# Performance work log

Measured on AMD Instinct MI355X. Metric: run time of the kernel, lower is better.

## Reference

```python
import jax, jax.numpy as jnp
import numpy as np

BATCH = 1024
INPUT_DIM = 4096
HIDDEN_DIM = 4096
N_BLOCKS = 8
BLOCK_SIZE = HIDDEN_DIM // N_BLOCKS          # 512
IN_BLOCK_SIZE = INPUT_DIM // N_BLOCKS        # 512


def setup_inputs() -> dict:
    key = jax.random.key(0)
    ks = jax.random.split(key, 6)
    scale = 1.0 / np.sqrt(BLOCK_SIZE)  # torch GRUCell init: U(-1/sqrt(hidden), 1/sqrt(hidden))
    return {
        "x": jax.random.normal(ks[0], (BATCH, INPUT_DIM), dtype=jnp.float32),
        "h": jax.random.normal(ks[1], (BATCH, HIDDEN_DIM), dtype=jnp.float32),
        "W_ih": jax.random.normal(ks[2], (N_BLOCKS, 3 * BLOCK_SIZE, IN_BLOCK_SIZE), dtype=jnp.float32) * scale,
        "W_hh": jax.random.normal(ks[3], (N_BLOCKS, 3 * BLOCK_SIZE, BLOCK_SIZE), dtype=jnp.float32) * scale,
        "b_ih": jax.random.normal(ks[4], (N_BLOCKS, 3 * BLOCK_SIZE), dtype=jnp.float32) * scale,
        "b_hh": jax.random.normal(ks[5], (N_BLOCKS, 3 * BLOCK_SIZE), dtype=jnp.float32) * scale,
    }


def reference(x, h, W_ih, W_hh, b_ih, b_hh):
    B = x.shape[0]
    n, g3, ibs = W_ih.shape           # n_blocks, 3*block_size, input_block_size
    bs = W_hh.shape[2]                # block_size
    xb = x.reshape(B, n, ibs)         # (B, n_blocks, input_block_size)
    hb = h.reshape(B, n, bs)          # (B, n_blocks, block_size)
    # Block-diagonal GEMM: one grouped matmul over all blocks at once.
    gi = jnp.einsum('bni,ngi->bng', xb, W_ih) + b_ih   # (B, n, 3*bs)
    gh = jnp.einsum('bnh,ngh->bng', hb, W_hh) + b_hh   # (B, n, 3*bs)
    i_r, i_z, i_n = jnp.split(gi, 3, axis=-1)
    h_r, h_z, h_n = jnp.split(gh, 3, axis=-1)
    r = jax.nn.sigmoid(i_r + h_r)                      # reset gate
    z = jax.nn.sigmoid(i_z + h_z)                      # update gate
    n_gate = jnp.tanh(i_n + r * h_n)                   # candidate state
    new_h = n_gate + z * (hb - n_gate)                 # torch GRUCell: h' = (1-z)*n + z*h
    return new_h.reshape(B, n * bs)
```

## Files before the change

### kernel.cpp

```cpp
#include <hip/hip_runtime.h>
#include <hip/hip_bf16.h>
#include <stdint.h>

#define G1CAST(p) ((const __attribute__((address_space(1))) void*)(p))
#define L3CAST(p) ((__attribute__((address_space(3))) void*)(p))

typedef short bf16x8 __attribute__((ext_vector_type(8)));
typedef float f32x16 __attribute__((ext_vector_type(16)));

static __device__ __forceinline__ short f2bf(float f) {
    __hip_bfloat16 b = __float2bfloat16(f);
    return __builtin_bit_cast(short, b);
}

__global__ __launch_bounds__(256) void wconv_kernel(const float* __restrict__ Wih,
                                                    const float* __restrict__ Whh,
                                                    short* __restrict__ Wstep) {
    const int b = blockIdx.x;
    const int vb = (b & 7) * 768 + (b >> 3);
    const int gid = vb * 256 + threadIdx.x;
    const int lane = gid & 63;
    int t1 = gid >> 6;
    const int g = t1 % 3;  t1 /= 3;
    const int wn = t1 & 1; t1 >>= 1;
    const int s = t1 & 63; t1 >>= 6;
    const int jt = t1 & 7;
    const int nblk = t1 >> 3;
    const int j = jt * 64 + wn * 32 + (lane & 31);
    const int kk = s * 16 + (lane >> 5) * 8;
    const float* src = (kk < 512)
        ? Wih + ((int64_t)nblk * 786432 + (int64_t)(g * 512 + j) * 512 + kk)
        : Whh + ((int64_t)nblk * 786432 + (int64_t)(g * 512 + j) * 512 + (kk - 512));
    const float4 a = ((const float4*)src)[0];
    const float4 bq = ((const float4*)src)[1];
    bf16x8 o;
    o[0] = f2bf(a.x); o[1] = f2bf(a.y); o[2] = f2bf(a.z); o[3] = f2bf(a.w);
    o[4] = f2bf(bq.x); o[5] = f2bf(bq.y); o[6] = f2bf(bq.z); o[7] = f2bf(bq.w);
    *(bf16x8*)(Wstep + (size_t)gid * 8) = o;
}

__global__ __launch_bounds__(256) void aconv_kernel(const float* __restrict__ x,
                                                    const float* __restrict__ h,
                                                    short* __restrict__ Afrag) {
    const int b = blockIdx.x;
    const int n = b & 7;
    const int inner = b >> 3;
    const int rb = inner >> 4;
    const int u = inner & 15;
    const int tid = threadIdx.x;
    const int lane = tid & 63;
    const int s = u * 4 + (tid >> 6);
    const int row = rb * 32 + (lane & 31);
    const int kk = s * 16 + (lane >> 5) * 8;
    const float* src = (kk < 512)
        ? x + ((size_t)row * 4096 + n * 512 + kk)
        : h + ((size_t)row * 4096 + n * 512 + (kk - 512));
    const float4 a = ((const float4*)src)[0];
    const float4 bq = ((const float4*)src)[1];
    bf16x8 o;
    o[0] = f2bf(a.x); o[1] = f2bf(a.y); o[2] = f2bf(a.z); o[3] = f2bf(a.w);
    o[4] = f2bf(bq.x); o[5] = f2bf(bq.y); o[6] = f2bf(bq.z); o[7] = f2bf(bq.w);
    const size_t dst = ((((size_t)(rb * 8 + n) * 64 + s) * 64) + lane) * 8;
    *(bf16x8*)(Afrag + dst) = o;
}

__global__ __launch_bounds__(256, 4) void gru_kernel(
    const float* __restrict__ hst,
    const short* __restrict__ Wstep, const short* __restrict__ Afrag,
    const float* __restrict__ b_ih, const float* __restrict__ b_hh,
    float* __restrict__ out)
{
    __shared__ __align__(16) char ldsB[4][8192];

    const int tid = threadIdx.x;
    const int nblk = blockIdx.x & 7;
    const int rr_ = blockIdx.x >> 3;
    const int jt = rr_ & 7;
    const int bt = rr_ >> 3;
    const int brow0 = bt * 64;

    const int lane = tid & 63;
    const int wave = tid >> 6;
    const int wm = wave >> 1;
    const int wn = wave & 1;
    const int l31 = lane & 31;
    const int k8 = lane >> 5;

    const int d0 = wave * 2048;
    const int ssrc0 = (d0 >= 6144) ? d0 - 6144 : d0;
    const int ssrc1 = (d0 + 1024 >= 6144) ? d0 + 1024 - 6144 : d0 + 1024;
    const char* wstep0 = (const char*)Wstep + (size_t)((nblk * 8 + jt) * 64) * 6144
                       + (size_t)lane * 16;
    const char* ab = (const char*)Afrag
        + ((size_t)((bt * 2 + wm) * 8 + nblk) << 16) + (size_t)lane * 16;
    const int boff = (wn * 3) * 1024 + lane * 16;

    f32x16 acc_r = {};
    f32x16 acc_z = {};
    f32x16 acc_nx = {};
    f32x16 acc_nh = {};

    bf16x8 aP, aQ, aR, aS;

#define LDA(T, s_v)                                                        \
    {                                                                      \
        const int sc = (s_v) > 63 ? 63 : (s_v);                            \
        a##T = *(const bf16x8*)(ab + (size_t)sc * 1024);                   \
    }

    auto stageB = [&](int s, int slot) {
        const int sc = s > 63 ? 63 : s;
        const char* src = wstep0 + (size_t)sc * 6144;
        char* dst = (char*)&ldsB[slot][0] + d0;
        __builtin_amdgcn_global_load_lds(G1CAST(src + ssrc0), L3CAST(dst), 16, 0, 0);
        __builtin_amdgcn_global_load_lds(G1CAST(src + ssrc1), L3CAST(dst + 1024), 16, 0, 0);
    };

#define ITER(C, L, accN)                                                            \
    {                                                                               \
        __builtin_amdgcn_s_barrier();                                               \
        stageB(s_ + 3, (s_ + 3) & 3);                                               \
        LDA(L, s_ + 3)                                                              \
        __builtin_amdgcn_sched_barrier(0);                                          \
        asm volatile("s_waitcnt vmcnt(6)" ::: "memory");                            \
        const char* bp = &ldsB[s_ & 3][boff];                                       \
        bf16x8 b0 = *(const bf16x8*)(bp);                                           \
        bf16x8 b1 = *(const bf16x8*)(bp + 1024);                                    \
        bf16x8 b2 = *(const bf16x8*)(bp + 2048);                                    \
        __builtin_amdgcn_s_setprio(1);                                              \
        acc_r = __builtin_amdgcn_mfma_f32_32x32x16_bf16(a##C, b0, acc_r, 0, 0, 0);  \
        acc_z = __builtin_amdgcn_mfma_f32_32x32x16_bf16(a##C, b1, acc_z, 0, 0, 0);  \
        accN  = __builtin_amdgcn_mfma_f32_32x32x16_bf16(a##C, b2, accN, 0, 0, 0);   \
        __builtin_amdgcn_s_setprio(0);                                              \
        s_ += 1;                                                                    \
    }

    stageB(0, 0); stageB(1, 1); stageB(2, 2);
    LDA(P, 0) LDA(Q, 1) LDA(R, 2)

    int s_ = 0;

    #pragma unroll 1
    for (int g4 = 0; g4 < 8; ++g4) {
        ITER(P, S, acc_nx)
        ITER(Q, P, acc_nx)
        ITER(R, Q, acc_nx)
        ITER(S, R, acc_nx)
    }
    #pragma unroll 1
    for (int g4 = 0; g4 < 8; ++g4) {
        ITER(P, S, acc_nh)
        ITER(Q, P, acc_nh)
        ITER(R, Q, acc_nh)
        ITER(S, R, acc_nh)
    }
#undef ITER
#undef LDA

    const int jb = jt * 64 + wn * 32 + l31;
    const int bb = nblk * 1536 + jb;
    const float br = b_ih[bb] + b_hh[bb];
    const float bz = b_ih[bb + 512] + b_hh[bb + 512];
    const float bnx = b_ih[bb + 1024];
    const float bnh = b_hh[bb + 1024];
    const int gcol = nblk * 512 + jb;
    #pragma unroll
    for (int rr = 0; rr < 16; ++rr) {
        const int rowl = (rr & 3) + 8 * (rr >> 2) + 4 * k8;
        const int row = brow0 + wm * 32 + rowl;
        const size_t idx = (size_t)row * 4096 + gcol;
        const float sr = acc_r[rr] + br;
        const float sz = acc_z[rr] + bz;
        const float rg = 1.f / (1.f + __expf(-sr));
        const float zg = 1.f / (1.f + __expf(-sz));
        const float tin = (acc_nx[rr] + bnx) + rg * (acc_nh[rr] + bnh);
        const float e2 = __expf(-2.f * tin);
        const float ng = 2.f / (1.f + e2) - 1.f;
        const float hv = hst[idx];
        out[idx] = ng + zg * (hv - ng);
    }
}

extern "C" void kernel_launch(void* const* d_in, const int* in_sizes, int n_in,
                              void* d_out, int out_size, void* d_ws, size_t ws_size,
                              hipStream_t stream) {
    (void)in_sizes; (void)n_in; (void)out_size; (void)ws_size;
    const float* x    = (const float*)d_in[0];
    const float* h    = (const float*)d_in[1];
    const float* W_ih = (const float*)d_in[2];
    const float* W_hh = (const float*)d_in[3];
    const float* b_ih = (const float*)d_in[4];
    const float* b_hh = (const float*)d_in[5];
    short* Wstep = (short*)d_ws;
    short* Afrag = (short*)d_ws + (size_t)12 * 1024 * 1024;

    wconv_kernel<<<6144, 256, 0, stream>>>(W_ih, W_hh, Wstep);
    aconv_kernel<<<4096, 256, 0, stream>>>(x, h, Afrag);
    gru_kernel<<<1024, 256, 0, stream>>>(h, Wstep, Afrag, b_ih, b_hh, (float*)d_out);
}
```

Measured before the change: 63.75 us.

## Deepen GRU GEMM pipeline to six LDS stages with register-prefetched B fragments

Grows the LDS ring buffer for weight tiles from 4 to 6 stages and prefetches B fragments from LDS into registers two steps ahead, so each MFMA uses operands loaded earlier. The wait on global-to-LDS loads moves before the barrier and the loop rotates register sets by explicit offsets. The goal is to hide global and LDS latency behind the matrix ops. In exchange LDS use per block rises to 48KB and the occupancy hint drops to 3 blocks per CU, with more register pressure from the extra fragment registers.

```diff
diff --git a/kernel.cpp b/kernel.cpp
--- a/kernel.cpp
+++ b/kernel.cpp
@@ -64,13 +64,13 @@
     *(bf16x8*)(Afrag + dst) = o;
 }
 
-__global__ __launch_bounds__(256, 4) void gru_kernel(
+__global__ __launch_bounds__(256, 3) void gru_kernel(
     const float* __restrict__ hst,
     const short* __restrict__ Wstep, const short* __restrict__ Afrag,
     const float* __restrict__ b_ih, const float* __restrict__ b_hh,
     float* __restrict__ out)
 {
-    __shared__ __align__(16) char ldsB[4][8192];
+    __shared__ __align__(16) char ldsB[6][8192];
 
     const int tid = threadIdx.x;
     const int nblk = blockIdx.x & 7;
@@ -94,66 +94,86 @@
     const char* ab = (const char*)Afrag
         + ((size_t)((bt * 2 + wm) * 8 + nblk) << 16) + (size_t)lane * 16;
     const int boff = (wn * 3) * 1024 + lane * 16;
+    const char* ldsBase = &ldsB[0][0];
 
     f32x16 acc_r = {};
     f32x16 acc_z = {};
     f32x16 acc_nx = {};
     f32x16 acc_nh = {};
 
-    bf16x8 aP, aQ, aR, aS;
+    bf16x8 a_0, a_1, a_2, a_3;
+    bf16x8 b0_0, b1_0, b2_0, b0_1, b1_1, b2_1;
+    bf16x8 b0_2, b1_2, b2_2, b0_3, b1_3, b2_3;
 
 #define LDA(T, s_v)                                                        \
     {                                                                      \
         const int sc = (s_v) > 63 ? 63 : (s_v);                            \
-        a##T = *(const bf16x8*)(ab + (size_t)sc * 1024);                   \
-    }
-
-    auto stageB = [&](int s, int slot) {
+        a_##T = *(const bf16x8*)(ab + (size_t)sc * 1024);                  \
+    }
+
+    auto stageB = [&](int s, int off) {
         const int sc = s > 63 ? 63 : s;
         const char* src = wstep0 + (size_t)sc * 6144;
-        char* dst = (char*)&ldsB[slot][0] + d0;
+        char* dst = (char*)ldsBase + off + d0;
         __builtin_amdgcn_global_load_lds(G1CAST(src + ssrc0), L3CAST(dst), 16, 0, 0);
         __builtin_amdgcn_global_load_lds(G1CAST(src + ssrc1), L3CAST(dst + 1024), 16, 0, 0);
     };
 
-#define ITER(C, L, accN)                                                            \
+#define ITER(AC, AL, BU, BR, accN)                                                  \
     {                                                                               \
+        asm volatile("s_waitcnt vmcnt(4)" ::: "memory");                            \
         __builtin_amdgcn_s_barrier();                                               \
-        stageB(s_ + 3, (s_ + 3) & 3);                                               \
-        LDA(L, s_ + 3)                                                              \
-        __builtin_amdgcn_sched_barrier(0);                                          \
-        asm volatile("s_waitcnt vmcnt(6)" ::: "memory");                            \
-        const char* bp = &ldsB[s_ & 3][boff];                                       \
-        bf16x8 b0 = *(const bf16x8*)(bp);                                           \
-        bf16x8 b1 = *(const bf16x8*)(bp + 1024);                                    \
-        bf16x8 b2 = *(const bf16x8*)(bp + 2048);                                    \
+        const char* rp = ldsBase + rdoff + boff;                                    \
+        b0_##BR = *(const bf16x8*)(rp);                                             \
+        b1_##BR = *(const bf16x8*)(rp + 1024);                                      \
+        b2_##BR = *(const bf16x8*)(rp + 2048);                                      \
+        stageB(s_ + 5, stoff);                                                      \
+        LDA(AL, s_ + 3)                                                             \
         __builtin_amdgcn_s_setprio(1);                                              \
-        acc_r = __builtin_amdgcn_mfma_f32_32x32x16_bf16(a##C, b0, acc_r, 0, 0, 0);  \
-        acc_z = __builtin_amdgcn_mfma_f32_32x32x16_bf16(a##C, b1, acc_z, 0, 0, 0);  \
-        accN  = __builtin_amdgcn_mfma_f32_32x32x16_bf16(a##C, b2, accN, 0, 0, 0);   \
+        acc_r = __builtin_amdgcn_mfma_f32_32x32x16_bf16(a_##AC, b0_##BU, acc_r, 0, 0, 0); \
+        acc_z = __builtin_amdgcn_mfma_f32_32x32x16_bf16(a_##AC, b1_##BU, acc_z, 0, 0, 0); \
+        accN  = __builtin_amdgcn_mfma_f32_32x32x16_bf16(a_##AC, b2_##BU, accN, 0, 0, 0);  \
         __builtin_amdgcn_s_setprio(0);                                              \
+        rdoff += 8192; if (rdoff >= 49152) rdoff -= 49152;                          \
+        stoff += 8192; if (stoff >= 49152) stoff -= 49152;                          \
         s_ += 1;                                                                    \
     }
 
-    stageB(0, 0); stageB(1, 1); stageB(2, 2);
-    LDA(P, 0) LDA(Q, 1) LDA(R, 2)
+#define GROUP(accN)          \
+    ITER(0, 3, 0, 2, accN)   \
+    ITER(1, 0, 1, 3, accN)   \
+    ITER(2, 1, 2, 0, accN)   \
+    ITER(3, 2, 3, 1, accN)
+
+    LDA(0, 0) LDA(1, 1) LDA(2, 2)
+    stageB(0, 0); stageB(1, 8192); stageB(2, 16384);
+    stageB(3, 24576); stageB(4, 32768);
+    asm volatile("s_waitcnt vmcnt(4)" ::: "memory");
+    __builtin_amdgcn_s_barrier();
+    {
+        const char* rp0 = ldsBase + boff;
+        b0_0 = *(const bf16x8*)(rp0);
+        b1_0 = *(const bf16x8*)(rp0 + 1024);
+        b2_0 = *(const bf16x8*)(rp0 + 2048);
+        const char* rp1 = ldsBase + 8192 + boff;
+        b0_1 = *(const bf16x8*)(rp1);
+        b1_1 = *(const bf16x8*)(rp1 + 1024);
+        b2_1 = *(const bf16x8*)(rp1 + 2048);
+    }
 
     int s_ = 0;
+    int rdoff = 16384;
+    int stoff = 40960;
 
     #pragma unroll 1
-    for (int g4 = 0; g4 < 8; ++g4) {
-        ITER(P, S, acc_nx)
-        ITER(Q, P, acc_nx)
-        ITER(R, Q, acc_nx)
-        ITER(S, R, acc_nx)
+    for (int g8 = 0; g8 < 8; ++g8) {
+        GROUP(acc_nx)
     }
     #pragma unroll 1
-    for (int g4 = 0; g4 < 8; ++g4) {
-        ITER(P, S, acc_nh)
-        ITER(Q, P, acc_nh)
-        ITER(R, Q, acc_nh)
-        ITER(S, R, acc_nh)
-    }
+    for (int g8 = 0; g8 < 8; ++g8) {
+        GROUP(acc_nh)
+    }
+#undef GROUP
 #undef ITER
 #undef LDA
 
```

After: 69.92 us. 1.1x slower.

## Stage four K-steps per barrier with triple-buffered larger LDS tiles

Applied to the files above, without the earlier changes.

The GEMM main loop now stages four K-steps (24 KB of weights) per barrier into a 3-slot LDS ring, instead of one K-step per barrier with a 4-slot ring. A fragments are double-buffered in registers, four at a time. This cuts the barrier and waitcnt count by 4x and issues larger batches of loads. The cost is 72 KB of LDS per block and launch bounds lowered to 2 blocks per CU, which reduces occupancy and latency hiding.

```diff
diff --git a/kernel.cpp b/kernel.cpp
--- a/kernel.cpp
+++ b/kernel.cpp
@@ -64,13 +64,13 @@
     *(bf16x8*)(Afrag + dst) = o;
 }
 
-__global__ __launch_bounds__(256, 4) void gru_kernel(
+__global__ __launch_bounds__(256, 2) void gru_kernel(
     const float* __restrict__ hst,
     const short* __restrict__ Wstep, const short* __restrict__ Afrag,
     const float* __restrict__ b_ih, const float* __restrict__ b_hh,
     float* __restrict__ out)
 {
-    __shared__ __align__(16) char ldsB[4][8192];
+    __shared__ __align__(16) char ldsB[3][24576];
 
     const int tid = threadIdx.x;
     const int nblk = blockIdx.x & 7;
@@ -86,11 +86,9 @@
     const int l31 = lane & 31;
     const int k8 = lane >> 5;
 
-    const int d0 = wave * 2048;
-    const int ssrc0 = (d0 >= 6144) ? d0 - 6144 : d0;
-    const int ssrc1 = (d0 + 1024 >= 6144) ? d0 + 1024 - 6144 : d0 + 1024;
     const char* wstep0 = (const char*)Wstep + (size_t)((nblk * 8 + jt) * 64) * 6144
-                       + (size_t)lane * 16;
+                       + (size_t)wave * 6144 + (size_t)lane * 16;
+    const int bdst0 = wave * 6144 + lane * 16;
     const char* ab = (const char*)Afrag
         + ((size_t)((bt * 2 + wm) * 8 + nblk) << 16) + (size_t)lane * 16;
     const int boff = (wn * 3) * 1024 + lane * 16;
@@ -100,62 +98,74 @@
     f32x16 acc_nx = {};
     f32x16 acc_nh = {};
 
-    bf16x8 aP, aQ, aR, aS;
-
-#define LDA(T, s_v)                                                        \
+    bf16x8 aC0, aC1, aC2, aC3, aN0, aN1, aN2, aN3;
+
+#define LDA4(T, it)                                                        \
     {                                                                      \
-        const int sc = (s_v) > 63 ? 63 : (s_v);                            \
-        a##T = *(const bf16x8*)(ab + (size_t)sc * 1024);                   \
-    }
-
-    auto stageB = [&](int s, int slot) {
-        const int sc = s > 63 ? 63 : s;
-        const char* src = wstep0 + (size_t)sc * 6144;
-        char* dst = (char*)&ldsB[slot][0] + d0;
-        __builtin_amdgcn_global_load_lds(G1CAST(src + ssrc0), L3CAST(dst), 16, 0, 0);
-        __builtin_amdgcn_global_load_lds(G1CAST(src + ssrc1), L3CAST(dst + 1024), 16, 0, 0);
+        const int ic = (it) > 15 ? 15 : (it);                              \
+        const char* ap = ab + (size_t)(ic * 4) * 1024;                     \
+        a##T##0 = *(const bf16x8*)(ap);                                    \
+        a##T##1 = *(const bf16x8*)(ap + 1024);                             \
+        a##T##2 = *(const bf16x8*)(ap + 2048);                             \
+        a##T##3 = *(const bf16x8*)(ap + 3072);                             \
+    }
+
+    auto stageB = [&](int it, int slot) {
+        const int ic = it > 15 ? 15 : it;
+        const char* src = wstep0 + (size_t)(ic * 4) * 6144;
+        char* dst = (char*)&ldsB[slot][0] + bdst0;
+        #pragma unroll
+        for (int c = 0; c < 6; ++c)
+            __builtin_amdgcn_global_load_lds(G1CAST(src + c * 1024),
+                                             L3CAST(dst + c * 1024), 16, 0, 0);
     };
 
-#define ITER(C, L, accN)                                                            \
+#define SUBSTEP(T, u, accN)                                                         \
     {                                                                               \
-        __builtin_amdgcn_s_barrier();                                               \
-        stageB(s_ + 3, (s_ + 3) & 3);                                               \
-        LDA(L, s_ + 3)                                                              \
-        __builtin_amdgcn_sched_barrier(0);                                          \
-        asm volatile("s_waitcnt vmcnt(6)" ::: "memory");                            \
-        const char* bp = &ldsB[s_ & 3][boff];                                       \
+        const char* bp = (const char*)&ldsB[0][0] + rdoff + (u) * 6144 + boff;      \
         bf16x8 b0 = *(const bf16x8*)(bp);                                           \
         bf16x8 b1 = *(const bf16x8*)(bp + 1024);                                    \
         bf16x8 b2 = *(const bf16x8*)(bp + 2048);                                    \
-        __builtin_amdgcn_s_setprio(1);                                              \
-        acc_r = __builtin_amdgcn_mfma_f32_32x32x16_bf16(a##C, b0, acc_r, 0, 0, 0);  \
-        acc_z = __builtin_amdgcn_mfma_f32_32x32x16_bf16(a##C, b1, acc_z, 0, 0, 0);  \
-        accN  = __builtin_amdgcn_mfma_f32_32x32x16_bf16(a##C, b2, accN, 0, 0, 0);   \
-        __builtin_amdgcn_s_setprio(0);                                              \
-        s_ += 1;                                                                    \
-    }
-
-    stageB(0, 0); stageB(1, 1); stageB(2, 2);
-    LDA(P, 0) LDA(Q, 1) LDA(R, 2)
-
-    int s_ = 0;
+        acc_r = __builtin_amdgcn_mfma_f32_32x32x16_bf16(a##T##u, b0, acc_r, 0, 0, 0); \
+        acc_z = __builtin_amdgcn_mfma_f32_32x32x16_bf16(a##T##u, b1, acc_z, 0, 0, 0); \
+        accN  = __builtin_amdgcn_mfma_f32_32x32x16_bf16(a##T##u, b2, accN, 0, 0, 0);  \
+    }
+
+#define ITER(T, O, accN)                                                            \
+    {                                                                               \
+        asm volatile("s_waitcnt vmcnt(10)" ::: "memory");                           \
+        __builtin_amdgcn_s_barrier();                                               \
+        stageB(i_ + 2, stslot);                                                     \
+        LDA4(O, i_ + 1)                                                             \
+        SUBSTEP(T, 0, accN)                                                         \
+        SUBSTEP(T, 1, accN)                                                         \
+        SUBSTEP(T, 2, accN)                                                         \
+        SUBSTEP(T, 3, accN)                                                         \
+        rdoff += 24576; if (rdoff >= 73728) rdoff -= 73728;                         \
+        stslot = (stslot == 2) ? 0 : stslot + 1;                                    \
+        i_ += 1;                                                                    \
+    }
+
+    stageB(0, 0); stageB(1, 1);
+    LDA4(C, 0)
+
+    int i_ = 0;
+    int rdoff = 0;
+    int stslot = 2;
 
     #pragma unroll 1
-    for (int g4 = 0; g4 < 8; ++g4) {
-        ITER(P, S, acc_nx)
-        ITER(Q, P, acc_nx)
-        ITER(R, Q, acc_nx)
-        ITER(S, R, acc_nx)
+    for (int g2 = 0; g2 < 4; ++g2) {
+        ITER(C, N, acc_nx)
+        ITER(N, C, acc_nx)
     }
     #pragma unroll 1
-    for (int g4 = 0; g4 < 8; ++g4) {
-        ITER(P, S, acc_nh)
-        ITER(Q, P, acc_nh)
-        ITER(R, Q, acc_nh)
-        ITER(S, R, acc_nh)
+    for (int g2 = 0; g2 < 4; ++g2) {
+        ITER(C, N, acc_nh)
+        ITER(N, C, acc_nh)
     }
 #undef ITER
-#undef LDA
+#undef SUBSTEP
+#undef LDA4
 
     const int jb = jt * 64 + wn * 32 + l31;
     const int bb = nblk * 1536 + jb;
```

Result: no change. 63.76 us (+0.0%).
